# Performance work log

Hardware: AMD Instinct MI355X
Metric: run time of the kernel (lower is better)

The kernel has to match this reference:

```python
import jax, jax.numpy as jnp
import numpy as np

D = 768
H = 12
HD = D // H
EPS = 1e-8  # torch cosine_similarity default eps


def setup_inputs() -> dict:
    key = jax.random.key(0)
    ks = jax.random.split(key, 16)
    bs, T, K = 8, 2048, 512
    s = 0.02
    return {
        "hidden_states": jax.random.normal(ks[0], (bs, T, D), jnp.float32),
        "attention_mask": jnp.ones((bs, T), jnp.int32),
        "pooled_hidden_states": jax.random.normal(ks[1], (bs, D), jnp.float32),
        "kg_key": jax.random.normal(ks[2], (bs, K, D), jnp.float32),
        "kg_value": jax.random.normal(ks[3], (bs, K, D), jnp.float32),
        "beta": jnp.ones((H,), jnp.float32),
        "Wq": jax.random.normal(ks[4], (D, D), jnp.float32) * s,
        "bq": jnp.zeros((D,), jnp.float32),
        "Wk": jax.random.normal(ks[5], (D, D), jnp.float32) * s,
        "bk": jnp.zeros((D,), jnp.float32),
        "Wv": jax.random.normal(ks[6], (D, D), jnp.float32) * s,
        "bv": jnp.zeros((D,), jnp.float32),
        "Wo": jax.random.normal(ks[7], (D, D), jnp.float32) * s,
        "bo": jnp.zeros((D,), jnp.float32),
    }


def reference(hidden_states, attention_mask, pooled_hidden_states, kg_key, kg_value,
              beta, Wq, bq, Wk, bk, Wv, bv, Wo, bo):
    bs, T, _ = hidden_states.shape
    K = kg_key.shape[1]
    # cosine similarity between pooled state and each KG key: [bs, K]
    pn = pooled_hidden_states / jnp.maximum(
        jnp.linalg.norm(pooled_hidden_states, axis=-1, keepdims=True), EPS)
    kn = kg_key / jnp.maximum(jnp.linalg.norm(kg_key, axis=-1, keepdims=True), EPS)
    sim = jnp.einsum("bd,bkd->bk", pn, kn)

    scale = HD ** -0.5
    # projections (torch Linear: y = x @ W.T + b)
    q = ((hidden_states @ Wq.T + bq) * scale).reshape(bs, T, H, HD).transpose(0, 2, 1, 3)
    k = (kg_value @ Wk.T + bk).reshape(bs, K, H, HD).transpose(0, 2, 1, 3)
    v = (kg_value @ Wv.T + bv).reshape(bs, K, H, HD).transpose(0, 2, 1, 3)

    # scores + per-head cosine-sim bias: [bs, H, T, K]
    scores = jnp.einsum("bhtd,bhkd->bhtk", q, k)
    scores = scores + beta[None, :, None, None] * sim[:, None, None, :]
    probs = jax.nn.softmax(scores, axis=-1)

    out = jnp.einsum("bhtk,bhkd->bhtd", probs, v)
    out = out.transpose(0, 2, 1, 3).reshape(bs, T, D)
    return out @ Wo.T + bo
```

## Files before the change

kernel.cpp:

```cpp
#include <hip/hip_runtime.h>
#include <math.h>

#define D_MODEL 768
#define NHEAD   12
#define HD      64
#define SEQ_T   2048
#define SEQ_K   512
#define BS      8
#define EPS_COS 1e-8f
#define LOG2E   1.44269504f

typedef short  bf16x8 __attribute__((ext_vector_type(8)));
typedef float  f32x4  __attribute__((ext_vector_type(4)));

__device__ __forceinline__ ushort f2bf(float x) {
    unsigned b = __float_as_uint(x);
    return (ushort)((b + 0x7FFF + ((b >> 16) & 1)) >> 16);
}
__device__ __forceinline__ unsigned cvt_pk_bf16(float lo, float hi) {
    unsigned r;
    asm("v_cvt_pk_bf16_f32 %0, %1, %2" : "=v"(r) : "v"(lo), "v"(hi));
    return r;
}
__device__ __forceinline__ float exp2_fast(float x) {
    float r;
    asm("v_exp_f32 %0, %1" : "=v"(r) : "v"(x));
    return r;
}

__device__ __forceinline__ void async_copy16(void* lds_base, const void* g_src) {
    __builtin_amdgcn_global_load_lds(
        (const __attribute__((address_space(1))) unsigned int*)g_src,
        (__attribute__((address_space(3))) unsigned int*)lds_base,
        16, 0, 0);
}

__global__ __launch_bounds__(256) void cvt4_kernel(
    const float* __restrict__ s0, const float* __restrict__ s1,
    const float* __restrict__ s2, const float* __restrict__ s3,
    ushort* __restrict__ d0, ushort* __restrict__ d1,
    ushort* __restrict__ d2, ushort* __restrict__ d3)
{
    const float* s; ushort* d;
    switch (blockIdx.y) {
        case 0: s = s0; d = d0; break;
        case 1: s = s1; d = d1; break;
        case 2: s = s2; d = d2; break;
        default: s = s3; d = d3; break;
    }
    int i = blockIdx.x * 256 + threadIdx.x;
    float4 v = reinterpret_cast<const float4*>(s)[i];
    ushort4 o;
    o.x = f2bf(v.x); o.y = f2bf(v.y); o.z = f2bf(v.z); o.w = f2bf(v.w);
    reinterpret_cast<ushort4*>(d)[i] = o;
}

__global__ __launch_bounds__(256, 3) void fused_proj_sim_kernel(
    const float* __restrict__ hidden, const float* __restrict__ kg_val,
    const ushort* __restrict__ Wqb, const float* __restrict__ bq,
    const ushort* __restrict__ Wkb, const float* __restrict__ bk_,
    const ushort* __restrict__ Wvb, const float* __restrict__ bv_,
    const float* __restrict__ pooled, const float* __restrict__ kg_key,
    const float* __restrict__ beta,
    ushort* __restrict__ qout, ushort* __restrict__ kout,
    ushort* __restrict__ vtout, float* __restrict__ bsim, float qscale)
{
    __shared__ __align__(16) char lds[49152];
    constexpr int Kd = D_MODEL;
    const int bid = blockIdx.x;
    const int tid = threadIdx.x, wid = tid >> 6, l = tid & 63;
    const int g = l >> 4, c = l & 15;

    if (bid < 768) {
        float*  AsF = (float*)lds;
        ushort* Bs  = (ushort*)(lds + 32768);
        const int m0 = (bid & 127) * 128, n0 = (bid >> 7) * 128;
        const int wm = (wid >> 1) * 64, wn = (wid & 1) * 64;

        f32x4 acc[4][4] = {};
        for (int k0 = 0; k0 < Kd; k0 += 64) {
            __syncthreads();
#pragma unroll
            for (int it = 0; it < 8; ++it) {
                int L = wid * 8192 + it * 1024 + l * 16;
                int row = L >> 8;
                int blk = (L >> 4) & 15;
                int gb = (blk & 8) | ((blk & 7) ^ (row & 7));
                async_copy16((char*)AsF + wid * 8192 + it * 1024,
                             hidden + (size_t)(m0 + row) * Kd + k0 + gb * 4);
            }
#pragma unroll
            for (int it = 0; it < 4; ++it) {
                int L = wid * 4096 + it * 1024 + l * 16;
                int row = L >> 7;
                int gb = ((L >> 4) & 7) ^ (row & 7);
                async_copy16((char*)Bs + wid * 4096 + it * 1024,
                             Wqb + (size_t)(n0 + row) * Kd + k0 + gb * 8);
            }
            __syncthreads();

            bf16x8 af[4][2], bf[4][2];
#pragma unroll
            for (int mt = 0; mt < 4; ++mt)
#pragma unroll
                for (int ks = 0; ks < 2; ++ks) {
                    int row = wm + mt * 16 + c;
                    int b0 = ks * 8 + 2 * g;
                    int p0 = (b0 & 8) | ((b0 & 7) ^ (row & 7));
                    int p1 = (b0 & 8) | (((b0 + 1) & 7) ^ (row & 7));
                    f32x4 a0 = *(const f32x4*)((const char*)AsF + row * 256 + (p0 << 4));
                    f32x4 a1 = *(const f32x4*)((const char*)AsF + row * 256 + (p1 << 4));
                    union { unsigned u[4]; bf16x8 v; } t;
                    t.u[0] = cvt_pk_bf16(a0[0], a0[1]);
                    t.u[1] = cvt_pk_bf16(a0[2], a0[3]);
                    t.u[2] = cvt_pk_bf16(a1[0], a1[1]);
                    t.u[3] = cvt_pk_bf16(a1[2], a1[3]);
                    af[mt][ks] = t.v;
                }
#pragma unroll
            for (int nt = 0; nt < 4; ++nt)
#pragma unroll
                for (int ks = 0; ks < 2; ++ks) {
                    int row = wn + nt * 16 + c;
                    bf[nt][ks] = *(const bf16x8*)((const char*)Bs + row * 128 +
                                                  (((ks * 4 + g) ^ (row & 7)) << 4));
                }
            __builtin_amdgcn_s_setprio(1);
#pragma unroll
            for (int mt = 0; mt < 4; ++mt)
#pragma unroll
                for (int nt = 0; nt < 4; ++nt) {
                    acc[mt][nt] = __builtin_amdgcn_mfma_f32_16x16x32_bf16(
                        af[mt][0], bf[nt][0], acc[mt][nt], 0, 0, 0);
                    acc[mt][nt] = __builtin_amdgcn_mfma_f32_16x16x32_bf16(
                        af[mt][1], bf[nt][1], acc[mt][nt], 0, 0, 0);
                }
            __builtin_amdgcn_s_setprio(0);
        }
#pragma unroll
        for (int mt = 0; mt < 4; ++mt)
#pragma unroll
            for (int nt = 0; nt < 4; ++nt) {
                int col = n0 + wn + nt * 16 + c;
                float bv = bq[col];
#pragma unroll
                for (int j = 0; j < 4; ++j) {
                    int row = m0 + wm + mt * 16 + g * 4 + j;
                    qout[(size_t)row * Kd + col] = f2bf((acc[mt][nt][j] + bv) * qscale);
                }
            }
    } else if (bid < 1536) {
        float*  AsF = (float*)lds;
        ushort* Bk  = (ushort*)(lds + 16384);
        ushort* Bv  = (ushort*)(lds + 24576);
        const int q = bid - 768;
        const int m0 = (q & 63) * 64, h = q >> 6, n0 = h * 64;
        const int wm = (wid >> 1) * 32, wn = (wid & 1) * 32;

        f32x4 acck[2][2] = {}, accv[2][2] = {};
        for (int k0 = 0; k0 < Kd; k0 += 64) {
            __syncthreads();
#pragma unroll
            for (int it = 0; it < 4; ++it) {
                int L = wid * 4096 + it * 1024 + l * 16;
                int row = L >> 8;
                int blk = (L >> 4) & 15;
                int gb = (blk & 8) | ((blk & 7) ^ (row & 7));
                async_copy16((char*)AsF + wid * 4096 + it * 1024,
                             kg_val + (size_t)(m0 + row) * Kd + k0 + gb * 4);
            }
#pragma unroll
            for (int it = 0; it < 2; ++it) {
                int L = wid * 2048 + it * 1024 + l * 16;
                int row = L >> 7;
                int gb = ((L >> 4) & 7) ^ (row & 7);
                async_copy16((char*)Bk + wid * 2048 + it * 1024,
                             Wkb + (size_t)(n0 + row) * Kd + k0 + gb * 8);
                async_copy16((char*)Bv + wid * 2048 + it * 1024,
                             Wvb + (size_t)(n0 + row) * Kd + k0 + gb * 8);
            }
            __syncthreads();

            bf16x8 af[2][2], bkf[2][2], bvf[2][2];
#pragma unroll
            for (int mt = 0; mt < 2; ++mt)
#pragma unroll
                for (int ks = 0; ks < 2; ++ks) {
                    int row = wm + mt * 16 + c;
                    int b0 = ks * 8 + 2 * g;
                    int p0 = (b0 & 8) | ((b0 & 7) ^ (row & 7));
                    int p1 = (b0 & 8) | (((b0 + 1) & 7) ^ (row & 7));
                    f32x4 a0 = *(const f32x4*)((const char*)AsF + row * 256 + (p0 << 4));
                    f32x4 a1 = *(const f32x4*)((const char*)AsF + row * 256 + (p1 << 4));
                    union { unsigned u[4]; bf16x8 v; } t;
                    t.u[0] = cvt_pk_bf16(a0[0], a0[1]);
                    t.u[1] = cvt_pk_bf16(a0[2], a0[3]);
                    t.u[2] = cvt_pk_bf16(a1[0], a1[1]);
                    t.u[3] = cvt_pk_bf16(a1[2], a1[3]);
                    af[mt][ks] = t.v;
                }
#pragma unroll
            for (int nt = 0; nt < 2; ++nt)
#pragma unroll
                for (int ks = 0; ks < 2; ++ks) {
                    int row = wn + nt * 16 + c;
                    int off = row * 128 + (((ks * 4 + g) ^ (row & 7)) << 4);
                    bkf[nt][ks] = *(const bf16x8*)((const char*)Bk + off);
                    bvf[nt][ks] = *(const bf16x8*)((const char*)Bv + off);
                }
            __builtin_amdgcn_s_setprio(1);
#pragma unroll
            for (int mt = 0; mt < 2; ++mt)
#pragma unroll
                for (int nt = 0; nt < 2; ++nt)
#pragma unroll
                    for (int ks = 0; ks < 2; ++ks) {
                        acck[mt][nt] = __builtin_amdgcn_mfma_f32_16x16x32_bf16(
                            af[mt][ks], bkf[nt][ks], acck[mt][nt], 0, 0, 0);
                        accv[mt][nt] = __builtin_amdgcn_mfma_f32_16x16x32_bf16(
                            af[mt][ks], bvf[nt][ks], accv[mt][nt], 0, 0, 0);
                    }
            __builtin_amdgcn_s_setprio(0);
        }
#pragma unroll
        for (int mt = 0; mt < 2; ++mt)
#pragma unroll
            for (int nt = 0; nt < 2; ++nt) {
                int col = n0 + wn + nt * 16 + c;
                float bbk = bk_[col];
#pragma unroll
                for (int j = 0; j < 4; ++j) {
                    int row = m0 + wm + mt * 16 + 4 * g + j;
                    kout[(size_t)row * Kd + col] = f2bf(acck[mt][nt][j] + bbk);
                }
            }
        {
            int b = m0 >> 9;
            int kc = (m0 >> 7) & 3;
#pragma unroll
            for (int mt = 0; mt < 2; ++mt) {
                int kb0 = (m0 & 64) + wm + mt * 16 + 4 * g;
                int kp0 = ((kb0 >> 5) << 5) | (((kb0 >> 2) & 3) << 3) | (((kb0 >> 4) & 1) << 2);
#pragma unroll
                for (int nt = 0; nt < 2; ++nt) {
                    int d = wn + nt * 16 + c;
                    float bbv = bv_[n0 + d];
                    unsigned u0 = cvt_pk_bf16(accv[mt][nt][0] + bbv, accv[mt][nt][1] + bbv);
                    unsigned u1 = cvt_pk_bf16(accv[mt][nt][2] + bbv, accv[mt][nt][3] + bbv);
                    size_t base = ((size_t)(b * NHEAD + h) * HD + d) * SEQ_K + kc * 128 + kp0;
                    uint2 st2; st2.x = u0; st2.y = u1;
                    *(uint2*)(vtout + base) = st2;
                }
            }
        }
    } else {
        int wrow = (bid - 1536) * 4 + (tid >> 6);
        int lane = tid & 63;
        int b  = wrow >> 9;
        int kk = wrow & 511;
        const float* p   = pooled + (size_t)b * D_MODEL;
        const float* key = kg_key + ((size_t)b * SEQ_K + kk) * D_MODEL;
        float dpk = 0.f, dkk = 0.f, dpp = 0.f;
        for (int i = lane; i < D_MODEL; i += 64) {
            float pv = p[i], kv = key[i];
            dpk += pv * kv; dkk += kv * kv; dpp += pv * pv;
        }
        for (int off = 32; off; off >>= 1) {
            dpk += __shfl_xor(dpk, off);
            dkk += __shfl_xor(dkk, off);
            dpp += __shfl_xor(dpp, off);
        }
        if (lane == 0) {
            float np_ = fmaxf(sqrtf(dpp), EPS_COS);
            float nk_ = fmaxf(sqrtf(dkk), EPS_COS);
            float sv = (dpk / (np_ * nk_)) * LOG2E;
#pragma unroll
            for (int h = 0; h < NHEAD; ++h)
                bsim[(size_t)(b * NHEAD + h) * SEQ_K + kk] = beta[h] * sv;
        }
    }
}

__global__ __launch_bounds__(256, 2) void gemm_o_kernel(
    const ushort* __restrict__ A, const ushort* __restrict__ W,
    const float* __restrict__ bias, float* __restrict__ out_f32)
{
    constexpr int Kd = D_MODEL;
    __shared__ __align__(16) ushort As[128 * 64];
    __shared__ __align__(16) ushort Bs[128 * 64];
    const int tid = threadIdx.x, wid = tid >> 6, l = tid & 63;
    const int g = l >> 4, c = l & 15;
    const int m0 = blockIdx.x * 128, n0 = blockIdx.y * 128;
    const int wm = (wid >> 1) * 64, wn = (wid & 1) * 64;

    f32x4 acc[4][4] = {};

    for (int k0 = 0; k0 < Kd; k0 += 64) {
        __syncthreads();
#pragma unroll
        for (int it = 0; it < 4; ++it) {
            int L = wid * 4096 + it * 1024 + l * 16;
            int row = L >> 7;
            int gb = ((L >> 4) & 7) ^ (row & 7);
            async_copy16((char*)As + wid * 4096 + it * 1024,
                         A + (size_t)(m0 + row) * Kd + k0 + gb * 8);
        }
#pragma unroll
        for (int it = 0; it < 4; ++it) {
            int L = wid * 4096 + it * 1024 + l * 16;
            int row = L >> 7;
            int gb = ((L >> 4) & 7) ^ (row & 7);
            async_copy16((char*)Bs + wid * 4096 + it * 1024,
                         W + (size_t)(n0 + row) * Kd + k0 + gb * 8);
        }
        __syncthreads();

        bf16x8 af[4][2], bf[4][2];
#pragma unroll
        for (int mt = 0; mt < 4; ++mt)
#pragma unroll
            for (int ks = 0; ks < 2; ++ks) {
                int row = wm + mt * 16 + c;
                af[mt][ks] = *(const bf16x8*)((const char*)As + row * 128 +
                                              (((ks * 4 + g) ^ (row & 7)) << 4));
            }
#pragma unroll
        for (int nt = 0; nt < 4; ++nt)
#pragma unroll
            for (int ks = 0; ks < 2; ++ks) {
                int row = wn + nt * 16 + c;
                bf[nt][ks] = *(const bf16x8*)((const char*)Bs + row * 128 +
                                              (((ks * 4 + g) ^ (row & 7)) << 4));
            }
        __builtin_amdgcn_s_setprio(1);
#pragma unroll
        for (int mt = 0; mt < 4; ++mt)
#pragma unroll
            for (int nt = 0; nt < 4; ++nt) {
                acc[mt][nt] = __builtin_amdgcn_mfma_f32_16x16x32_bf16(
                    af[mt][0], bf[nt][0], acc[mt][nt], 0, 0, 0);
                acc[mt][nt] = __builtin_amdgcn_mfma_f32_16x16x32_bf16(
                    af[mt][1], bf[nt][1], acc[mt][nt], 0, 0, 0);
            }
        __builtin_amdgcn_s_setprio(0);
    }

#pragma unroll
    for (int mt = 0; mt < 4; ++mt)
#pragma unroll
        for (int nt = 0; nt < 4; ++nt) {
            int col = n0 + wn + nt * 16 + c;
            float bv = bias[col];
#pragma unroll
            for (int j = 0; j < 4; ++j) {
                int row = m0 + wm + mt * 16 + g * 4 + j;
                out_f32[(size_t)row * Kd + col] = acc[mt][nt][j] + bv;
            }
        }
}

__global__ __launch_bounds__(256, 4) void attn_mfma_kernel(
    const ushort* __restrict__ qb, const ushort* __restrict__ kbp,
    const ushort* __restrict__ vt, const float* __restrict__ bsim,
    ushort* __restrict__ ctx)
{
    int bid = blockIdx.x;
    int w = (bid & 7) * 192 + (bid >> 3);
    int tile = w & 15; int rest = w >> 4; int h = rest % 12; int b = rest / 12;
    int t0 = tile * 128;
    int tid = threadIdx.x, wid = tid >> 6, l = tid & 63;
    int g = l >> 4, c = l & 15;

    __shared__ __align__(16) char KV[2][16384];

    const ushort* srck[2]; const ushort* srcv[2];
    int offk[2], offv[2];
#pragma unroll
    for (int it = 0; it < 2; ++it) {
        int L = wid * 2048 + it * 1024 + l * 16;
        int row = L >> 7;
        int gb = ((L >> 4) & 7) ^ (row & 7);
        srck[it] = kbp + (size_t)(b * SEQ_K + row) * D_MODEL + h * HD + gb * 8;
        offk[it] = wid * 2048 + it * 1024;
        int d = row;
        int blk = (L >> 4) & 7;
        int gblk = blk ^ (d & 7);
        srcv[it] = vt + ((size_t)((b * NHEAD + h) * HD + d)) * SEQ_K + gblk * 8;
        offv[it] = 8192 + wid * 2048 + it * 1024;
    }

#pragma unroll
    for (int it = 0; it < 4; ++it) {
        int L = wid * 4096 + it * 1024 + l * 16;
        int row = L >> 7;
        int gb = ((L >> 4) & 7) ^ (row & 7);
        async_copy16(&KV[0][0] + wid * 4096 + it * 1024,
                     qb + (size_t)(b * SEQ_T + t0 + row) * D_MODEL + h * HD + gb * 8);
    }
    const float* bsrow = bsim + (size_t)(b * NHEAD + h) * SEQ_K;
    __syncthreads();

    bf16x8 aq[2][2];
#pragma unroll
    for (int sub = 0; sub < 2; ++sub)
#pragma unroll
        for (int ks = 0; ks < 2; ++ks) {
            int row = wid * 32 + sub * 16 + c;
            aq[sub][ks] = *(const bf16x8*)(&KV[0][0] + row * 128 +
                                           (((ks * 4 + g) ^ (row & 7)) << 4));
        }
    __syncthreads();

#pragma unroll
    for (int it = 0; it < 2; ++it) {
        async_copy16(&KV[0][0] + offk[it], srck[it]);
        async_copy16(&KV[0][0] + offv[it], srcv[it]);
    }

    const bf16x8 ones8 = {(short)0x3F80, (short)0x3F80, (short)0x3F80, (short)0x3F80,
                          (short)0x3F80, (short)0x3F80, (short)0x3F80, (short)0x3F80};
    f32x4 oacc[2][4] = {};
    f32x4 oSum[2] = {};
    int cur = 0;

    for (int kc = 0; kc < 8; ++kc) {
        __syncthreads();
        if (kc < 7) {
            int nxt = cur ^ 1;
#pragma unroll
            for (int it = 0; it < 2; ++it) {
                srck[it] += 64 * D_MODEL;
                async_copy16(&KV[nxt][0] + offk[it], srck[it]);
                srcv[it] += 64;
                async_copy16(&KV[nxt][0] + offv[it], srcv[it]);
            }
        }
        const char* Kb = &KV[cur][0];
        const char* Vb = &KV[cur][0] + 8192;

#pragma unroll
        for (int kb = 0; kb < 2; ++kb) {
            f32x4 st[2][2];
            __builtin_amdgcn_s_setprio(1);
#pragma unroll
            for (int n2 = 0; n2 < 2; ++n2) {
                int nt = 2 * kb + n2;
                f32x4 cinit = *(const f32x4*)(bsrow + kc * 64 + nt * 16 + 4 * g);
                int krow = nt * 16 + c;
                bf16x8 ak0 = *(const bf16x8*)(Kb + krow * 128 +
                                              ((g ^ (krow & 7)) << 4));
                bf16x8 ak1 = *(const bf16x8*)(Kb + krow * 128 +
                                              (((4 + g) ^ (krow & 7)) << 4));
#pragma unroll
                for (int sub = 0; sub < 2; ++sub) {
                    st[sub][n2] = __builtin_amdgcn_mfma_f32_16x16x32_bf16(
                        ak0, aq[sub][0], cinit, 0, 0, 0);
                    st[sub][n2] = __builtin_amdgcn_mfma_f32_16x16x32_bf16(
                        ak1, aq[sub][1], st[sub][n2], 0, 0, 0);
                }
            }
            __builtin_amdgcn_s_setprio(0);

            bf16x8 pa[2];
#pragma unroll
            for (int sub = 0; sub < 2; ++sub) {
                f32x4 e0, e1;
#pragma unroll
                for (int j = 0; j < 4; ++j) {
                    e0[j] = exp2_fast(st[sub][0][j]);
                    e1[j] = exp2_fast(st[sub][1][j]);
                }
                union { unsigned u[4]; bf16x8 v; } pk;
                pk.u[0] = cvt_pk_bf16(e0[0], e0[1]);
                pk.u[1] = cvt_pk_bf16(e0[2], e0[3]);
                pk.u[2] = cvt_pk_bf16(e1[0], e1[1]);
                pk.u[3] = cvt_pk_bf16(e1[2], e1[3]);
                pa[sub] = pk.v;
            }

            __builtin_amdgcn_s_setprio(1);
#pragma unroll
            for (int sub = 0; sub < 2; ++sub)
                oSum[sub] = __builtin_amdgcn_mfma_f32_16x16x32_bf16(
                    pa[sub], ones8, oSum[sub], 0, 0, 0);
#pragma unroll
            for (int dt = 0; dt < 4; ++dt) {
                int d = dt * 16 + c;
                int blk = kb * 4 + g;
                int sb = blk ^ (d & 7);
                bf16x8 bv = *(const bf16x8*)(Vb + d * 128 + (sb << 4));
#pragma unroll
                for (int sub = 0; sub < 2; ++sub)
                    oacc[sub][dt] = __builtin_amdgcn_mfma_f32_16x16x32_bf16(
                        pa[sub], bv, oacc[sub][dt], 0, 0, 0);
            }
            __builtin_amdgcn_s_setprio(0);
        }
        cur ^= 1;
    }

#pragma unroll
    for (int sub = 0; sub < 2; ++sub) {
        f32x4 invL;
#pragma unroll
        for (int j = 0; j < 4; ++j) invL[j] = 1.f / oSum[sub][j];
#pragma unroll
        for (int dt = 0; dt < 4; ++dt)
#pragma unroll
            for (int j = 0; j < 4; ++j) {
                int trow = t0 + wid * 32 + sub * 16 + 4 * g + j;
                int d = dt * 16 + c;
                ctx[(size_t)(b * SEQ_T + trow) * D_MODEL + h * HD + d] =
                    f2bf(oacc[sub][dt][j] * invL[j]);
            }
    }
}

extern "C" void kernel_launch(void* const* d_in, const int* in_sizes, int n_in,
                              void* d_out, int out_size, void* d_ws, size_t ws_size,
                              hipStream_t stream)
{
    const float* hidden  = (const float*)d_in[0];
    const float* pooled  = (const float*)d_in[2];
    const float* kg_key  = (const float*)d_in[3];
    const float* kg_val  = (const float*)d_in[4];
    const float* beta    = (const float*)d_in[5];
    const float* Wq = (const float*)d_in[6];  const float* bq = (const float*)d_in[7];
    const float* Wk = (const float*)d_in[8];  const float* bk = (const float*)d_in[9];
    const float* Wv = (const float*)d_in[10]; const float* bv = (const float*)d_in[11];
    const float* Wo = (const float*)d_in[12]; const float* bo = (const float*)d_in[13];
    float* out = (float*)d_out;

    const size_t MQ = (size_t)BS * SEQ_T;
    const size_t MK = (size_t)BS * SEQ_K;
    const size_t DW = D_MODEL * D_MODEL;

    float*  bsim = (float*)d_ws;
    ushort* wqb  = (ushort*)(bsim + BS * NHEAD * SEQ_K);
    ushort* wkb  = wqb + DW;
    ushort* wvb  = wkb + DW;
    ushort* wob  = wvb + DW;
    ushort* qbb  = wob + DW;
    ushort* kbb  = qbb + MQ * D_MODEL;
    ushort* vtb  = kbb + MK * D_MODEL;
    ushort* ctxb = vtb + MK * D_MODEL;

    cvt4_kernel<<<dim3(DW / 4 / 256, 4), 256, 0, stream>>>(
        Wq, Wk, Wv, Wo, wqb, wkb, wvb, wob);

    fused_proj_sim_kernel<<<2560, 256, 0, stream>>>(
        hidden, kg_val, wqb, bq, wkb, bk, wvb, bv,
        pooled, kg_key, beta, qbb, kbb, vtb, bsim, 0.125f * LOG2E);

    attn_mfma_kernel<<<BS * NHEAD * (SEQ_T / 128), 256, 0, stream>>>(
        qbb, kbb, vtb, bsim, ctxb);

    gemm_o_kernel<<<dim3(MQ / 128, 6), 256, 0, stream>>>(ctxb, wob, bo, out);
}
```

Measured before the change: 118.3 us.

## Split fused projection/similarity kernel into separate Q, KV and sim kernels

```diff
diff --git a/kernel.cpp b/kernel.cpp
--- a/kernel.cpp
+++ b/kernel.cpp
@@ -55,228 +55,236 @@
     reinterpret_cast<ushort4*>(d)[i] = o;
 }
 
-__global__ __launch_bounds__(256, 3) void fused_proj_sim_kernel(
-    const float* __restrict__ hidden, const float* __restrict__ kg_val,
-    const ushort* __restrict__ Wqb, const float* __restrict__ bq,
-    const ushort* __restrict__ Wkb, const float* __restrict__ bk_,
-    const ushort* __restrict__ Wvb, const float* __restrict__ bv_,
+__global__ __launch_bounds__(256) void sim_kernel(
     const float* __restrict__ pooled, const float* __restrict__ kg_key,
-    const float* __restrict__ beta,
-    ushort* __restrict__ qout, ushort* __restrict__ kout,
-    ushort* __restrict__ vtout, float* __restrict__ bsim, float qscale)
-{
-    __shared__ __align__(16) char lds[49152];
+    const float* __restrict__ beta, float* __restrict__ bsim)
+{
+    int wid  = (blockIdx.x * blockDim.x + threadIdx.x) >> 6;
+    int lane = threadIdx.x & 63;
+    int b  = wid >> 9;
+    int kk = wid & 511;
+    const float* p   = pooled + (size_t)b * D_MODEL;
+    const float* key = kg_key + ((size_t)b * SEQ_K + kk) * D_MODEL;
+    float dpk = 0.f, dkk = 0.f, dpp = 0.f;
+    for (int i = lane; i < D_MODEL; i += 64) {
+        float pv = p[i], kv = key[i];
+        dpk += pv * kv; dkk += kv * kv; dpp += pv * pv;
+    }
+    for (int off = 32; off; off >>= 1) {
+        dpk += __shfl_xor(dpk, off);
+        dkk += __shfl_xor(dkk, off);
+        dpp += __shfl_xor(dpp, off);
+    }
+    if (lane == 0) {
+        float np_ = fmaxf(sqrtf(dpp), EPS_COS);
+        float nk_ = fmaxf(sqrtf(dkk), EPS_COS);
+        float sv = (dpk / (np_ * nk_)) * LOG2E;
+#pragma unroll
+        for (int h = 0; h < NHEAD; ++h)
+            bsim[(size_t)(b * NHEAD + h) * SEQ_K + kk] = beta[h] * sv;
+    }
+}
+
+__global__ __launch_bounds__(256, 3) void gemm_q_a32_kernel(
+    const float* __restrict__ A, const ushort* __restrict__ W,
+    const float* __restrict__ bias, ushort* __restrict__ out_bf, float scale)
+{
     constexpr int Kd = D_MODEL;
-    const int bid = blockIdx.x;
+    __shared__ __align__(16) float  AsF[128 * 64];
+    __shared__ __align__(16) ushort Bs[128 * 64];
     const int tid = threadIdx.x, wid = tid >> 6, l = tid & 63;
     const int g = l >> 4, c = l & 15;
-
-    if (bid < 768) {
-        float*  AsF = (float*)lds;
-        ushort* Bs  = (ushort*)(lds + 32768);
-        const int m0 = (bid & 127) * 128, n0 = (bid >> 7) * 128;
-        const int wm = (wid >> 1) * 64, wn = (wid & 1) * 64;
-
-        f32x4 acc[4][4] = {};
-        for (int k0 = 0; k0 < Kd; k0 += 64) {
-            __syncthreads();
-#pragma unroll
-            for (int it = 0; it < 8; ++it) {
-                int L = wid * 8192 + it * 1024 + l * 16;
-                int row = L >> 8;
-                int blk = (L >> 4) & 15;
-                int gb = (blk & 8) | ((blk & 7) ^ (row & 7));
-                async_copy16((char*)AsF + wid * 8192 + it * 1024,
-                             hidden + (size_t)(m0 + row) * Kd + k0 + gb * 4);
-            }
-#pragma unroll
-            for (int it = 0; it < 4; ++it) {
-                int L = wid * 4096 + it * 1024 + l * 16;
-                int row = L >> 7;
-                int gb = ((L >> 4) & 7) ^ (row & 7);
-                async_copy16((char*)Bs + wid * 4096 + it * 1024,
-                             Wqb + (size_t)(n0 + row) * Kd + k0 + gb * 8);
-            }
-            __syncthreads();
-
-            bf16x8 af[4][2], bf[4][2];
-#pragma unroll
-            for (int mt = 0; mt < 4; ++mt)
+    const int m0 = blockIdx.x * 128, n0 = blockIdx.y * 128;
+    const int wm = (wid >> 1) * 64, wn = (wid & 1) * 64;
+
+    f32x4 acc[4][4] = {};
+
+    for (int k0 = 0; k0 < Kd; k0 += 64) {
+        __syncthreads();
+#pragma unroll
+        for (int it = 0; it < 8; ++it) {
+            int L = wid * 8192 + it * 1024 + l * 16;
+            int row = L >> 8;
+            int blk = (L >> 4) & 15;
+            int gb = (blk & 8) | ((blk & 7) ^ (row & 7));
+            async_copy16((char*)AsF + wid * 8192 + it * 1024,
+                         A + (size_t)(m0 + row) * Kd + k0 + gb * 4);
+        }
+#pragma unroll
+        for (int it = 0; it < 4; ++it) {
+            int L = wid * 4096 + it * 1024 + l * 16;
+            int row = L >> 7;
+            int gb = ((L >> 4) & 7) ^ (row & 7);
+            async_copy16((char*)Bs + wid * 4096 + it * 1024,
+                         W + (size_t)(n0 + row) * Kd + k0 + gb * 8);
+        }
+        __syncthreads();
+
+        bf16x8 af[4][2], bf[4][2];
+#pragma unroll
+        for (int mt = 0; mt < 4; ++mt)
+#pragma unroll
+            for (int ks = 0; ks < 2; ++ks) {
+                int row = wm + mt * 16 + c;
+                int b0 = ks * 8 + 2 * g;
+                int p0 = (b0 & 8) | ((b0 & 7) ^ (row & 7));
+                int p1 = (b0 & 8) | (((b0 + 1) & 7) ^ (row & 7));
+                f32x4 a0 = *(const f32x4*)((const char*)AsF + row * 256 + (p0 << 4));
+                f32x4 a1 = *(const f32x4*)((const char*)AsF + row * 256 + (p1 << 4));
+                union { unsigned u[4]; bf16x8 v; } t;
+                t.u[0] = cvt_pk_bf16(a0[0], a0[1]);
+                t.u[1] = cvt_pk_bf16(a0[2], a0[3]);
+                t.u[2] = cvt_pk_bf16(a1[0], a1[1]);
+                t.u[3] = cvt_pk_bf16(a1[2], a1[3]);
+                af[mt][ks] = t.v;
+            }
+#pragma unroll
+        for (int nt = 0; nt < 4; ++nt)
+#pragma unroll
+            for (int ks = 0; ks < 2; ++ks) {
+                int row = wn + nt * 16 + c;
+                bf[nt][ks] = *(const bf16x8*)((const char*)Bs + row * 128 +
+                                              (((ks * 4 + g) ^ (row & 7)) << 4));
+            }
+        __builtin_amdgcn_s_setprio(1);
+#pragma unroll
+        for (int mt = 0; mt < 4; ++mt)
+#pragma unroll
+            for (int nt = 0; nt < 4; ++nt) {
+                acc[mt][nt] = __builtin_amdgcn_mfma_f32_16x16x32_bf16(
+                    af[mt][0], bf[nt][0], acc[mt][nt], 0, 0, 0);
+                acc[mt][nt] = __builtin_amdgcn_mfma_f32_16x16x32_bf16(
+                    af[mt][1], bf[nt][1], acc[mt][nt], 0, 0, 0);
+            }
+        __builtin_amdgcn_s_setprio(0);
+    }
+
+#pragma unroll
+    for (int mt = 0; mt < 4; ++mt)
+#pragma unroll
+        for (int nt = 0; nt < 4; ++nt) {
+            int col = n0 + wn + nt * 16 + c;
+            float bv = bias[col];
+#pragma unroll
+            for (int j = 0; j < 4; ++j) {
+                int row = m0 + wm + mt * 16 + g * 4 + j;
+                out_bf[(size_t)row * Kd + col] = f2bf((acc[mt][nt][j] + bv) * scale);
+            }
+        }
+}
+
+__global__ __launch_bounds__(256, 3) void gemm_kv_a32_kernel(
+    const float* __restrict__ A,
+    const ushort* __restrict__ Wk_, const float* __restrict__ bk_,
+    const ushort* __restrict__ Wv_, const float* __restrict__ bv_,
+    ushort* __restrict__ outk, ushort* __restrict__ vt)
+{
+    constexpr int Kd = D_MODEL;
+    __shared__ __align__(16) float  AsF[64 * 64];
+    __shared__ __align__(16) ushort Bk[64 * 64];
+    __shared__ __align__(16) ushort Bv[64 * 64];
+    const int tid = threadIdx.x, wid = tid >> 6, l = tid & 63;
+    const int g = l >> 4, c = l & 15;
+    const int m0 = blockIdx.x * 64, h = blockIdx.y, n0 = h * 64;
+    const int wm = (wid >> 1) * 32, wn = (wid & 1) * 32;
+
+    f32x4 acck[2][2] = {}, accv[2][2] = {};
+
+    for (int k0 = 0; k0 < Kd; k0 += 64) {
+        __syncthreads();
+#pragma unroll
+        for (int it = 0; it < 4; ++it) {
+            int L = wid * 4096 + it * 1024 + l * 16;
+            int row = L >> 8;
+            int blk = (L >> 4) & 15;
+            int gb = (blk & 8) | ((blk & 7) ^ (row & 7));
+            async_copy16((char*)AsF + wid * 4096 + it * 1024,
+                         A + (size_t)(m0 + row) * Kd + k0 + gb * 4);
+        }
+#pragma unroll
+        for (int it = 0; it < 2; ++it) {
+            int L = wid * 2048 + it * 1024 + l * 16;
+            int row = L >> 7;
+            int gb = ((L >> 4) & 7) ^ (row & 7);
+            async_copy16((char*)Bk + wid * 2048 + it * 1024,
+                         Wk_ + (size_t)(n0 + row) * Kd + k0 + gb * 8);
+            async_copy16((char*)Bv + wid * 2048 + it * 1024,
+                         Wv_ + (size_t)(n0 + row) * Kd + k0 + gb * 8);
+        }
+        __syncthreads();
+
+        bf16x8 af[2][2], bkf[2][2], bvf[2][2];
+#pragma unroll
+        for (int mt = 0; mt < 2; ++mt)
+#pragma unroll
+            for (int ks = 0; ks < 2; ++ks) {
+                int row = wm + mt * 16 + c;
+                int b0 = ks * 8 + 2 * g;
+                int p0 = (b0 & 8) | ((b0 & 7) ^ (row & 7));
+                int p1 = (b0 & 8) | (((b0 + 1) & 7) ^ (row & 7));
+                f32x4 a0 = *(const f32x4*)((const char*)AsF + row * 256 + (p0 << 4));
+                f32x4 a1 = *(const f32x4*)((const char*)AsF + row * 256 + (p1 << 4));
+                union { unsigned u[4]; bf16x8 v; } t;
+                t.u[0] = cvt_pk_bf16(a0[0], a0[1]);
+                t.u[1] = cvt_pk_bf16(a0[2], a0[3]);
+                t.u[2] = cvt_pk_bf16(a1[0], a1[1]);
+                t.u[3] = cvt_pk_bf16(a1[2], a1[3]);
+                af[mt][ks] = t.v;
+            }
+#pragma unroll
+        for (int nt = 0; nt < 2; ++nt)
+#pragma unroll
+            for (int ks = 0; ks < 2; ++ks) {
+                int row = wn + nt * 16 + c;
+                int off = row * 128 + (((ks * 4 + g) ^ (row & 7)) << 4);
+                bkf[nt][ks] = *(const bf16x8*)((const char*)Bk + off);
+                bvf[nt][ks] = *(const bf16x8*)((const char*)Bv + off);
+            }
+        __builtin_amdgcn_s_setprio(1);
+#pragma unroll
+        for (int mt = 0; mt < 2; ++mt)
+#pragma unroll
+            for (int nt = 0; nt < 2; ++nt)
 #pragma unroll
                 for (int ks = 0; ks < 2; ++ks) {
-                    int row = wm + mt * 16 + c;
-                    int b0 = ks * 8 + 2 * g;
-                    int p0 = (b0 & 8) | ((b0 & 7) ^ (row & 7));
-                    int p1 = (b0 & 8) | (((b0 + 1) & 7) ^ (row & 7));
-                    f32x4 a0 = *(const f32x4*)((const char*)AsF + row * 256 + (p0 << 4));
-                    f32x4 a1 = *(const f32x4*)((const char*)AsF + row * 256 + (p1 << 4));
-                    union { unsigned u[4]; bf16x8 v; } t;
-                    t.u[0] = cvt_pk_bf16(a0[0], a0[1]);
-                    t.u[1] = cvt_pk_bf16(a0[2], a0[3]);
-                    t.u[2] = cvt_pk_bf16(a1[0], a1[1]);
-                    t.u[3] = cvt_pk_bf16(a1[2], a1[3]);
-                    af[mt][ks] = t.v;
+                    acck[mt][nt] = __builtin_amdgcn_mfma_f32_16x16x32_bf16(
+                        af[mt][ks], bkf[nt][ks], acck[mt][nt], 0, 0, 0);
+                    accv[mt][nt] = __builtin_amdgcn_mfma_f32_16x16x32_bf16(
+                        af[mt][ks], bvf[nt][ks], accv[mt][nt], 0, 0, 0);
                 }
-#pragma unroll
-            for (int nt = 0; nt < 4; ++nt)
-#pragma unroll
-                for (int ks = 0; ks < 2; ++ks) {
-                    int row = wn + nt * 16 + c;
-                    bf[nt][ks] = *(const bf16x8*)((const char*)Bs + row * 128 +
-                                                  (((ks * 4 + g) ^ (row & 7)) << 4));
-                }
-            __builtin_amdgcn_s_setprio(1);
-#pragma unroll
-            for (int mt = 0; mt < 4; ++mt)
-#pragma unroll
-                for (int nt = 0; nt < 4; ++nt) {
-                    acc[mt][nt] = __builtin_amdgcn_mfma_f32_16x16x32_bf16(
-                        af[mt][0], bf[nt][0], acc[mt][nt], 0, 0, 0);
-                    acc[mt][nt] = __builtin_amdgcn_mfma_f32_16x16x32_bf16(
-                        af[mt][1], bf[nt][1], acc[mt][nt], 0, 0, 0);
-                }
-            __builtin_amdgcn_s_setprio(0);
-        }
-#pragma unroll
-        for (int mt = 0; mt < 4; ++mt)
-#pragma unroll
-            for (int nt = 0; nt < 4; ++nt) {
-                int col = n0 + wn + nt * 16 + c;
-                float bv = bq[col];
-#pragma unroll
-                for (int j = 0; j < 4; ++j) {
-                    int row = m0 + wm + mt * 16 + g * 4 + j;
-                    qout[(size_t)row * Kd + col] = f2bf((acc[mt][nt][j] + bv) * qscale);
-                }
-            }
-    } else if (bid < 1536) {
-        float*  AsF = (float*)lds;
-        ushort* Bk  = (ushort*)(lds + 16384);
-        ushort* Bv  = (ushort*)(lds + 24576);
-        const int q = bid - 768;
-        const int m0 = (q & 63) * 64, h = q >> 6, n0 = h * 64;
-        const int wm = (wid >> 1) * 32, wn = (wid & 1) * 32;
-
-        f32x4 acck[2][2] = {}, accv[2][2] = {};
-        for (int k0 = 0; k0 < Kd; k0 += 64) {
-            __syncthreads();
-#pragma unroll
-            for (int it = 0; it < 4; ++it) {
-                int L = wid * 4096 + it * 1024 + l * 16;
-                int row = L >> 8;
-                int blk = (L >> 4) & 15;
-                int gb = (blk & 8) | ((blk & 7) ^ (row & 7));
-                async_copy16((char*)AsF + wid * 4096 + it * 1024,
-                             kg_val + (size_t)(m0 + row) * Kd + k0 + gb * 4);
-            }
-#pragma unroll
-            for (int it = 0; it < 2; ++it) {
-                int L = wid * 2048 + it * 1024 + l * 16;
-                int row = L >> 7;
-                int gb = ((L >> 4) & 7) ^ (row & 7);
-                async_copy16((char*)Bk + wid * 2048 + it * 1024,
-                             Wkb + (size_t)(n0 + row) * Kd + k0 + gb * 8);
-                async_copy16((char*)Bv + wid * 2048 + it * 1024,
-                             Wvb + (size_t)(n0 + row) * Kd + k0 + gb * 8);
-            }
-            __syncthreads();
-
-            bf16x8 af[2][2], bkf[2][2], bvf[2][2];
-#pragma unroll
-            for (int mt = 0; mt < 2; ++mt)
-#pragma unroll
-                for (int ks = 0; ks < 2; ++ks) {
-                    int row = wm + mt * 16 + c;
-                    int b0 = ks * 8 + 2 * g;
-                    int p0 = (b0 & 8) | ((b0 & 7) ^ (row & 7));
-                    int p1 = (b0 & 8) | (((b0 + 1) & 7) ^ (row & 7));
-                    f32x4 a0 = *(const f32x4*)((const char*)AsF + row * 256 + (p0 << 4));
-                    f32x4 a1 = *(const f32x4*)((const char*)AsF + row * 256 + (p1 << 4));
-                    union { unsigned u[4]; bf16x8 v; } t;
-                    t.u[0] = cvt_pk_bf16(a0[0], a0[1]);
-                    t.u[1] = cvt_pk_bf16(a0[2], a0[3]);
-                    t.u[2] = cvt_pk_bf16(a1[0], a1[1]);
-                    t.u[3] = cvt_pk_bf16(a1[2], a1[3]);
-                    af[mt][ks] = t.v;
-                }
-#pragma unroll
-            for (int nt = 0; nt < 2; ++nt)
-#pragma unroll
-                for (int ks = 0; ks < 2; ++ks) {
-                    int row = wn + nt * 16 + c;
-                    int off = row * 128 + (((ks * 4 + g) ^ (row & 7)) << 4);
-                    bkf[nt][ks] = *(const bf16x8*)((const char*)Bk + off);
-                    bvf[nt][ks] = *(const bf16x8*)((const char*)Bv + off);
-                }
-            __builtin_amdgcn_s_setprio(1);
-#pragma unroll
-            for (int mt = 0; mt < 2; ++mt)
-#pragma unroll
-                for (int nt = 0; nt < 2; ++nt)
-#pragma unroll
-                    for (int ks = 0; ks < 2; ++ks) {
-                        acck[mt][nt] = __builtin_amdgcn_mfma_f32_16x16x32_bf16(
-                            af[mt][ks], bkf[nt][ks], acck[mt][nt], 0, 0, 0);
-                        accv[mt][nt] = __builtin_amdgcn_mfma_f32_16x16x32_bf16(
-                            af[mt][ks], bvf[nt][ks], accv[mt][nt], 0, 0, 0);
-                    }
-            __builtin_amdgcn_s_setprio(0);
-        }
-#pragma unroll
-        for (int mt = 0; mt < 2; ++mt)
+        __builtin_amdgcn_s_setprio(0);
+    }
+
+#pragma unroll
+    for (int mt = 0; mt < 2; ++mt)
+#pragma unroll
+        for (int nt = 0; nt < 2; ++nt) {
+            int col = n0 + wn + nt * 16 + c;
+            float bbk = bk_[col];
+#pragma unroll
+            for (int j = 0; j < 4; ++j) {
+                int row = m0 + wm + mt * 16 + 4 * g + j;
+                outk[(size_t)row * Kd + col] = f2bf(acck[mt][nt][j] + bbk);
+            }
+        }
+
+    {
+        int b = m0 >> 9;
+        int kc = (m0 >> 7) & 3;
+#pragma unroll
+        for (int mt = 0; mt < 2; ++mt) {
+            int kb0 = (m0 & 64) + wm + mt * 16 + 4 * g;
+            int kp0 = ((kb0 >> 5) << 5) | (((kb0 >> 2) & 3) << 3) | (((kb0 >> 4) & 1) << 2);
 #pragma unroll
             for (int nt = 0; nt < 2; ++nt) {
-                int col = n0 + wn + nt * 16 + c;
-                float bbk = bk_[col];
-#pragma unroll
-                for (int j = 0; j < 4; ++j) {
-                    int row = m0 + wm + mt * 16 + 4 * g + j;
-                    kout[(size_t)row * Kd + col] = f2bf(acck[mt][nt][j] + bbk);
-                }
-            }
-        {
-            int b = m0 >> 9;
-            int kc = (m0 >> 7) & 3;
-#pragma unroll
-            for (int mt = 0; mt < 2; ++mt) {
-                int kb0 = (m0 & 64) + wm + mt * 16 + 4 * g;
-                int kp0 = ((kb0 >> 5) << 5) | (((kb0 >> 2) & 3) << 3) | (((kb0 >> 4) & 1) << 2);
-#pragma unroll
-                for (int nt = 0; nt < 2; ++nt) {
-                    int d = wn + nt * 16 + c;
-                    float bbv = bv_[n0 + d];
-                    unsigned u0 = cvt_pk_bf16(accv[mt][nt][0] + bbv, accv[mt][nt][1] + bbv);
-                    unsigned u1 = cvt_pk_bf16(accv[mt][nt][2] + bbv, accv[mt][nt][3] + bbv);
-                    size_t base = ((size_t)(b * NHEAD + h) * HD + d) * SEQ_K + kc * 128 + kp0;
-                    uint2 st2; st2.x = u0; st2.y = u1;
-                    *(uint2*)(vtout + base) = st2;
-                }
-            }
-        }
-    } else {
-        int wrow = (bid - 1536) * 4 + (tid >> 6);
-        int lane = tid & 63;
-        int b  = wrow >> 9;
-        int kk = wrow & 511;
-        const float* p   = pooled + (size_t)b * D_MODEL;
-        const float* key = kg_key + ((size_t)b * SEQ_K + kk) * D_MODEL;
-        float dpk = 0.f, dkk = 0.f, dpp = 0.f;
-        for (int i = lane; i < D_MODEL; i += 64) {
-            float pv = p[i], kv = key[i];
-            dpk += pv * kv; dkk += kv * kv; dpp += pv * pv;
-        }
-        for (int off = 32; off; off >>= 1) {
-            dpk += __shfl_xor(dpk, off);
-            dkk += __shfl_xor(dkk, off);
-            dpp += __shfl_xor(dpp, off);
-        }
-        if (lane == 0) {
-            float np_ = fmaxf(sqrtf(dpp), EPS_COS);
-            float nk_ = fmaxf(sqrtf(dkk), EPS_COS);
-            float sv = (dpk / (np_ * nk_)) * LOG2E;
-#pragma unroll
-            for (int h = 0; h < NHEAD; ++h)
-                bsim[(size_t)(b * NHEAD + h) * SEQ_K + kk] = beta[h] * sv;
+                int d = wn + nt * 16 + c;
+                float bbv = bv_[n0 + d];
+                unsigned u0 = cvt_pk_bf16(accv[mt][nt][0] + bbv, accv[mt][nt][1] + bbv);
+                unsigned u1 = cvt_pk_bf16(accv[mt][nt][2] + bbv, accv[mt][nt][3] + bbv);
+                size_t base = ((size_t)(b * NHEAD + h) * HD + d) * SEQ_K + kc * 128 + kp0;
+                uint2 st2; st2.x = u0; st2.y = u1;
+                *(uint2*)(vt + base) = st2;
+            }
         }
     }
 }
@@ -548,9 +556,12 @@
     cvt4_kernel<<<dim3(DW / 4 / 256, 4), 256, 0, stream>>>(
         Wq, Wk, Wv, Wo, wqb, wkb, wvb, wob);
 
-    fused_proj_sim_kernel<<<2560, 256, 0, stream>>>(
-        hidden, kg_val, wqb, bq, wkb, bk, wvb, bv,
-        pooled, kg_key, beta, qbb, kbb, vtb, bsim, 0.125f * LOG2E);
+    sim_kernel<<<(BS * SEQ_K) / 4, 256, 0, stream>>>(pooled, kg_key, beta, bsim);
+
+    gemm_q_a32_kernel<<<dim3(MQ / 128, 6), 256, 0, stream>>>(
+        hidden, wqb, bq, qbb, 0.125f * LOG2E);
+    gemm_kv_a32_kernel<<<dim3(MK / 64, 12), 256, 0, stream>>>(
+        kg_val, wkb, bk, wvb, bv, kbb, vtb);
 
     attn_mfma_kernel<<<BS * NHEAD * (SEQ_T / 128), 256, 0, stream>>>(
         qbb, kbb, vtb, bsim, ctxb);
```

Result: slower. 121.5 us (+2.8%).
